# Kernel tuning notes

Hardware: AMD Instinct MI355X
Metric: run time of the kernel (lower is better)

Reference implementation:

```python
import jax, jax.numpy as jnp
import numpy as np

B, T, D, NH, FF, L, NCLS, CELL = 4, 64, 128, 4, 512, 2, 7, 64
DIMS = (600, 342, 300)


def layernorm(x, g, b, eps=1e-5):
    m = jnp.mean(x, -1, keepdims=True)
    v = jnp.mean((x - m) ** 2, -1, keepdims=True)
    return (x - m) / jnp.sqrt(v + eps) * g + b


def mha(x, Wqkv, bqkv, Wo, bo):
    N, S, Dm = x.shape
    hd = Dm // NH
    q, k, v = jnp.split(x @ Wqkv + bqkv, 3, axis=-1)
    q = q.reshape(N, S, NH, hd).transpose(0, 2, 1, 3) / jnp.float32(hd) ** 0.5
    k = k.reshape(N, S, NH, hd).transpose(0, 2, 1, 3)
    v = v.reshape(N, S, NH, hd).transpose(0, 2, 1, 3)
    att = jax.nn.softmax(jnp.einsum('nhqd,nhkd->nhqk', q, k), axis=-1)
    o = jnp.einsum('nhqk,nhkd->nhqd', att, v).transpose(0, 2, 1, 3).reshape(N, S, Dm)
    return o @ Wo + bo


def _l2norm(x):
    return x / jnp.maximum(jnp.linalg.norm(x, axis=-1, keepdims=True), 1e-12)


def _model(x_text, x_vis, x_aud, Wp_text, bp_text, Wp_vis, bp_vis, Wp_aud, bp_aud,
           lang1, lang2, Wl1, bl1, Wl2, bl2, phase_text, phase_vis, phase_aud,
           t_Wqkv, t_bqkv, t_Wo, t_bo, t_g1, t_b1, t_W1, t_bf1, t_W2, t_bf2, t_g2, t_b2,
           meas_r, meas_i, fc_W1, fc_b1, fc_W2, fc_b2):
    b, t = x_text.shape[0], x_text.shape[1]
    # modality projections + ReLU
    reps = [jax.nn.relu(x @ W + bb) for x, W, bb in
            ((x_text, Wp_text, bp_text), (x_vis, Wp_vis, bp_vis), (x_aud, Wp_aud, bp_aud))]
    l1 = jnp.broadcast_to(lang1, (b, t, lang1.shape[-1]))
    l2 = jnp.broadcast_to(lang2, (b, t, lang2.shape[-1]))
    lrep1 = jax.nn.relu(l1 @ Wl1 + bl1)
    lrep2 = jax.nn.relu(l2 @ Wl2 + bl2)
    amps = [_l2norm(r) for r in reps]
    lamp1, lamp2 = _l2norm(lrep1), _l2norm(lrep2)
    # phase embedding: smask is all-ones so index is always 0 -> single learned phase vector
    phases = [jnp.broadcast_to(p, (b, t, D)) for p in (phase_text, phase_vis, phase_aud)]
    cmul = lambda ph, a: (a * jnp.cos(ph), a * jnp.sin(ph))
    pure = [cmul(ph, a) for ph, a in zip(phases, amps)]
    ls1 = cmul(phases[0], lamp1)
    ls2 = cmul(phases[0], lamp2)
    # Hadamard gate analog on (real, imag)
    s2 = jnp.float32(2.0) ** -0.5
    h1 = ((ls1[0] + ls1[1]) * s2, (ls1[0] - ls1[1]) * s2)
    h2 = ((ls2[0] + ls2[1]) * s2, (ls2[0] - ls2[1]) * s2)
    # CNOT-style entanglement: complex elementwise product, renormalized to a pure state
    er = h1[0] * h2[0] - h1[1] * h2[1]
    ei = h1[0] * h2[1] + h1[1] * h2[0]
    en = jnp.maximum(jnp.sqrt(jnp.sum(er * er + ei * ei, -1, keepdims=True)), 1e-12)
    ent = (er / en, ei / en)

    def outer(st):  # rho = v v^dagger, v = r + i*im
        r, i = st
        rr = jnp.einsum('btd,bte->btde', r, r) + jnp.einsum('btd,bte->btde', i, i)
        ri = jnp.einsum('btd,bte->btde', i, r) - jnp.einsum('btd,bte->btde', r, i)
        return rr, ri

    mats = [outer(s) for s in pure] + [outer(ent)]
    w = jnp.concatenate([jnp.linalg.norm(r, axis=-1, keepdims=True)
                         for r in reps + [lrep1]], -1)
    w = jax.nn.softmax(w, -1)  # [B,T,4]
    rho_r = sum(w[..., m:m + 1, None] * mats[m][0] for m in range(4))
    rho_i = sum(w[..., m:m + 1, None] * mats[m][1] for m in range(4))
    # seq blocks: same block applied independently per timestep to real and imag parts
    # -> vectorize the Python loop over T (and the real/imag pair) into one batch dim
    x = jnp.concatenate([rho_r, rho_i], 0).reshape(2 * b * t, D, D)
    for l in range(L):
        x = layernorm(x + mha(x, t_Wqkv[l], t_bqkv[l], t_Wo[l], t_bo[l]), t_g1[l], t_b1[l])
        x = layernorm(x + (jax.nn.relu(x @ t_W1[l] + t_bf1[l]) @ t_W2[l] + t_bf2[l]),
                      t_g2[l], t_b2[l])
    x = x.reshape(2, b, t, D, D)
    rho_r, rho_i = x[0], x[1]
    # quantum measurement: p_k = Re(v_k^dagger rho v_k), v_k normalized complex vectors
    mn = jnp.maximum(jnp.sqrt(jnp.sum(meas_r ** 2 + meas_i ** 2, -1, keepdims=True)), 1e-12)
    vr, vi = meas_r / mn, meas_i / mn  # [K=D, D]
    ar = jnp.einsum('btde,ke->btkd', rho_r, vr) - jnp.einsum('btde,ke->btkd', rho_i, vi)
    ai = jnp.einsum('btde,ke->btkd', rho_r, vi) + jnp.einsum('btde,ke->btkd', rho_i, vr)
    probs = jnp.einsum('kd,btkd->btk', vr, ar) + jnp.einsum('kd,btkd->btk', vi, ai)
    logits = jax.nn.relu(probs @ fc_W1 + fc_b1) @ fc_W2 + fc_b2
    return jax.nn.log_softmax(logits, -1)  # [B,T,NCLS]


def setup_inputs():
    key = jax.random.key(0)
    ks = iter(jax.random.split(key, 32))
    rn = lambda shape, s=0.05: jax.random.normal(next(ks), shape, dtype=jnp.float32) * s
    z = lambda shape: jnp.zeros(shape, jnp.float32)
    o = lambda shape: jnp.ones(shape, jnp.float32)
    return dict(
        x_text=rn((B, T, DIMS[0]), 1.0), x_vis=rn((B, T, DIMS[1]), 1.0), x_aud=rn((B, T, DIMS[2]), 1.0),
        Wp_text=rn((DIMS[0], D)), bp_text=z((D,)),
        Wp_vis=rn((DIMS[1], D)), bp_vis=z((D,)),
        Wp_aud=rn((DIMS[2], D)), bp_aud=z((D,)),
        lang1=rn((1, 1, DIMS[2]), 1.0), lang2=rn((1, 1, DIMS[2]), 1.0),
        Wl1=rn((DIMS[2], D)), bl1=z((D,)), Wl2=rn((DIMS[2], D)), bl2=z((D,)),
        phase_text=rn((D,), 1.0), phase_vis=rn((D,), 1.0), phase_aud=rn((D,), 1.0),
        t_Wqkv=rn((L, D, 3 * D)), t_bqkv=z((L, 3 * D)),
        t_Wo=rn((L, D, D)), t_bo=z((L, D)),
        t_g1=o((L, D)), t_b1=z((L, D)),
        t_W1=rn((L, D, FF)), t_bf1=z((L, FF)),
        t_W2=rn((L, FF, D)), t_bf2=z((L, D)),
        t_g2=o((L, D)), t_b2=z((L, D)),
        meas_r=rn((D, D), 1.0), meas_i=rn((D, D), 1.0),
        fc_W1=rn((D, CELL)), fc_b1=z((CELL,)), fc_W2=rn((CELL, NCLS)), fc_b2=z((NCLS,)),
    )


def reference(x_text, x_vis, x_aud, Wp_text, bp_text, Wp_vis, bp_vis, Wp_aud, bp_aud,
              lang1, lang2, Wl1, bl1, Wl2, bl2, phase_text, phase_vis, phase_aud,
              t_Wqkv, t_bqkv, t_Wo, t_bo, t_g1, t_b1, t_W1, t_bf1, t_W2, t_bf2, t_g2, t_b2,
              meas_r, meas_i, fc_W1, fc_b1, fc_W2, fc_b2):
    return _model(x_text, x_vis, x_aud, Wp_text, bp_text, Wp_vis, bp_vis, Wp_aud, bp_aud,
                  lang1, lang2, Wl1, bl1, Wl2, bl2, phase_text, phase_vis, phase_aud,
                  t_Wqkv, t_bqkv, t_Wo, t_bo, t_g1, t_b1, t_W1, t_bf1, t_W2, t_bf2, t_g2, t_b2,
                  meas_r, meas_i, fc_W1, fc_b1, fc_W2, fc_b2)
```

## Files before the change

kernel.cpp:

```cpp
#include <hip/hip_runtime.h>
#include <hip/hip_bf16.h>

typedef __hip_bfloat16 bf16;
typedef short short8 __attribute__((ext_vector_type(8)));
typedef float f32x4 __attribute__((ext_vector_type(4)));

__device__ __forceinline__ float b2f(bf16 v){ return __bfloat162float(v); }

__device__ __forceinline__ short f2bs(float f){
  union { __hip_bfloat16 b; short s; } u; u.b = __float2bfloat16(f); return u.s;
}
__device__ __forceinline__ float bs2f(short s){
  union { short s; __hip_bfloat16 b; } u; u.s = s; return __bfloat162float(u.b);
}

__device__ __forceinline__ float wred_sum(float v){
  #pragma unroll
  for (int o = 32; o > 0; o >>= 1) v += __shfl_xor(v, o, 64);
  return v;
}

__device__ __forceinline__ void gload_lds16(const void* g, void* l){
  __builtin_amdgcn_global_load_lds((const __attribute__((address_space(1))) unsigned*)g,
                                   (__attribute__((address_space(3))) unsigned*)l, 16, 0, 0);
}

__device__ __forceinline__ unsigned swzA(unsigned a){ return a ^ (((a >> 8) & 7u) << 4); }
__device__ __forceinline__ unsigned swzB(unsigned a){ return a ^ (((a >> 7) & 3u) << 4); }

template<int DIMN>
__device__ void modality(const float* x, const float* W, const float* bia, const float* ph,
                         float* PURE, float* RNORM, int m, int bt, float* xs, float* red)
{
  int tid = threadIdx.x;
  for (int i = tid; i < DIMN; i += 128) xs[i] = x[bt*DIMN + i];
  __syncthreads();
  float a0 = 0.f, a1 = 0.f, a2 = 0.f, a3 = 0.f;
  int k = 0;
  for (; k + 4 <= DIMN; k += 4){
    a0 = fmaf(xs[k],   W[(k  )*128 + tid], a0);
    a1 = fmaf(xs[k+1], W[(k+1)*128 + tid], a1);
    a2 = fmaf(xs[k+2], W[(k+2)*128 + tid], a2);
    a3 = fmaf(xs[k+3], W[(k+3)*128 + tid], a3);
  }
  for (; k < DIMN; k++) a0 = fmaf(xs[k], W[k*128 + tid], a0);
  float acc = bia[tid] + ((a0 + a1) + (a2 + a3));
  float rep = fmaxf(acc, 0.f);
  float s = wred_sum(rep*rep);
  int wid = tid >> 6, lane = tid & 63;
  if (lane == 0) red[wid] = s;
  __syncthreads();
  float nrm = sqrtf(red[0] + red[1]);
  float amp = rep / fmaxf(nrm, 1e-12f);
  float p = ph[tid];
  PURE[bt*768 + m*128 + tid]       = amp * cosf(p);
  PURE[bt*768 + (3+m)*128 + tid]   = amp * sinf(p);
  if (tid == 0) RNORM[bt*4 + m] = nrm;
}

__global__ void prep_kernel(
    const float* __restrict__ Wqkv, const float* __restrict__ Wo,
    const float* __restrict__ W1, const float* __restrict__ W2,
    short* __restrict__ WqkvT, short* __restrict__ WoT,
    short* __restrict__ W1T, short* __restrict__ W2T,
    const float* xt, const float* xv, const float* xa,
    const float* Wpt, const float* bpt, const float* Wpv, const float* bpv,
    const float* Wpa, const float* bpa,
    const float* pht, const float* phv, const float* pha,
    float* PURE, float* RNORM,
    const float* l1, const float* l2,
    const float* Wl1, const float* bl1, const float* Wl2, const float* bl2,
    float* LANGB,
    const float* mr, const float* mi, float* VMEAS, short* VMEASB)
{
  __shared__ float xs[600];
  __shared__ float xs2a[300];
  __shared__ float red[4];
  int b = blockIdx.x, tid = threadIdx.x;

  if (b < 384){
    int l = b / 192, bb = b - l*192;
    const float* in; short* out; int K, N, boff;
    bool isW2 = false;
    if (bb < 48)      { in = Wqkv; out = WqkvT; K = 128; N = 384; boff = bb; }
    else if (bb < 64) { in = Wo;   out = WoT;   K = 128; N = 128; boff = bb - 48; }
    else if (bb < 128){ in = W1;   out = W1T;   K = 128; N = 512; boff = bb - 64; }
    else              { in = W2;   out = W2T;   K = 512; N = 128; boff = bb - 128; isW2 = true; }
    int base = l * K * N;
    int i0 = boff * 1024;
    #pragma unroll
    for (int t = 0; t < 8; t++){
      int i = i0 + t*128 + tid;
      if (i < K*N){
        int nn = i / K, kk = i - nn*K;
        int oi = isW2 ? ((kk >> 5)*4096 + nn*32 + (kk & 31)) : i;
        out[base + oi] = f2bs(in[base + kk*N + nn]);
      }
    }
    return;
  }
  if (b < 1152){
    int idx = b - 384;
    int bt = idx & 255, m = idx >> 8;
    if (m == 0)      modality<600>(xt, Wpt, bpt, pht, PURE, RNORM, 0, bt, xs, red);
    else if (m == 1) modality<342>(xv, Wpv, bpv, phv, PURE, RNORM, 1, bt, xs, red);
    else             modality<300>(xa, Wpa, bpa, pha, PURE, RNORM, 2, bt, xs, red);
    return;
  }
  if (b >= 1153){
    int k = b - 1153;
    float a = mr[k*128 + tid], bb2 = mi[k*128 + tid];
    float ws = wred_sum(a*a + bb2*bb2);
    int wid = tid >> 6, lane = tid & 63;
    if (lane == 0) red[wid] = ws;
    __syncthreads();
    float inv = 1.f / fmaxf(sqrtf(red[0] + red[1]), 1e-12f);
    float vr = a * inv, vi = bb2 * inv;
    int i = k*128 + tid;
    VMEAS[i]          = vr;
    VMEAS[16384 + i]  = vi;
    VMEASB[i]         = f2bs(vr);
    VMEASB[16384 + i] = f2bs(vi);
    VMEASB[32768 + i] = f2bs(-vi);
    return;
  }
  for (int i = tid; i < 300; i += 128){ xs[i] = l1[i]; xs2a[i] = l2[i]; }
  __syncthreads();
  float p10=0,p11=0,p12=0,p13=0, p20=0,p21=0,p22=0,p23=0;
  for (int k = 0; k < 300; k += 4){
    p10 = fmaf(xs[k],    Wl1[(k  )*128+tid], p10);
    p11 = fmaf(xs[k+1],  Wl1[(k+1)*128+tid], p11);
    p12 = fmaf(xs[k+2],  Wl1[(k+2)*128+tid], p12);
    p13 = fmaf(xs[k+3],  Wl1[(k+3)*128+tid], p13);
    p20 = fmaf(xs2a[k],  Wl2[(k  )*128+tid], p20);
    p21 = fmaf(xs2a[k+1],Wl2[(k+1)*128+tid], p21);
    p22 = fmaf(xs2a[k+2],Wl2[(k+2)*128+tid], p22);
    p23 = fmaf(xs2a[k+3],Wl2[(k+3)*128+tid], p23);
  }
  float a1 = bl1[tid] + ((p10+p11)+(p12+p13));
  float a2 = bl2[tid] + ((p20+p21)+(p22+p23));
  a1 = fmaxf(a1, 0.f); a2 = fmaxf(a2, 0.f);
  int wid = tid >> 6, lane = tid & 63;
  float s1 = wred_sum(a1*a1), s2 = wred_sum(a2*a2);
  if (lane == 0){ red[wid] = s1; red[2+wid] = s2; }
  __syncthreads();
  float n1 = sqrtf(red[0] + red[1]);
  float n2 = sqrtf(red[2] + red[3]);
  float lamp1 = a1 / fmaxf(n1, 1e-12f);
  float lamp2 = a2 / fmaxf(n2, 1e-12f);
  float ph = pht[tid];
  float c = cosf(ph), s = sinf(ph);
  const float s2c = 0.70710678118654752f;
  float h1r = (lamp1*c + lamp1*s)*s2c, h1i = (lamp1*c - lamp1*s)*s2c;
  float h2r = (lamp2*c + lamp2*s)*s2c, h2i = (lamp2*c - lamp2*s)*s2c;
  float er = h1r*h2r - h1i*h2i;
  float ei = h1r*h2i + h1i*h2r;
  __syncthreads();
  float se = wred_sum(er*er + ei*ei);
  if (lane == 0) red[wid] = se;
  __syncthreads();
  float en = fmaxf(sqrtf(red[0] + red[1]), 1e-12f);
  LANGB[tid]       = er / en;
  LANGB[128 + tid] = ei / en;
  if (tid == 0) LANGB[256] = n1;
}

__global__ __launch_bounds__(256) void rho_kernel(const float* PURE, const float* RNORM,
                                                  const float* LANGB, short* Xb)
{
  __shared__ float rv[4][128], iv[4][128], wsm[4];
  int bt = blockIdx.x >> 1, half = blockIdx.x & 1;
  int tid = threadIdx.x;
  for (int i = tid; i < 1024; i += 256){
    int d = i & 127;
    if (i < 768){ int m = i >> 7; float v = PURE[bt*768 + i];
                  if (m < 3) rv[m][d] = v; else iv[m-3][d] = v; }
    else if (i < 896) rv[3][d] = LANGB[d];
    else              iv[3][d] = LANGB[128 + d];
  }
  if (tid == 0){
    float n0 = RNORM[bt*4+0], n1 = RNORM[bt*4+1], n2 = RNORM[bt*4+2], n3 = LANGB[256];
    float mx = fmaxf(fmaxf(n0, n1), fmaxf(n2, n3));
    float e0 = __expf(n0-mx), e1 = __expf(n1-mx), e2 = __expf(n2-mx), e3 = __expf(n3-mx);
    float inv = 1.f / (e0+e1+e2+e3);
    wsm[0]=e0*inv; wsm[1]=e1*inv; wsm[2]=e2*inv; wsm[3]=e3*inv;
  }
  __syncthreads();
  float w0 = wsm[0], w1 = wsm[1], w2 = wsm[2], w3 = wsm[3];
  int lo = half*8192, hi = lo + 8192;
  for (int idx = lo + tid; idx < hi; idx += 256){
    int d = idx >> 7, e = idx & 127;
    float rr = 0.f, ri = 0.f;
    {
      float rd=rv[0][d], re=rv[0][e], id=iv[0][d], ie=iv[0][e];
      rr = fmaf(w0, rd*re + id*ie, rr); ri = fmaf(w0, id*re - rd*ie, ri);
    }{
      float rd=rv[1][d], re=rv[1][e], id=iv[1][d], ie=iv[1][e];
      rr = fmaf(w1, rd*re + id*ie, rr); ri = fmaf(w1, id*re - rd*ie, ri);
    }{
      float rd=rv[2][d], re=rv[2][e], id=iv[2][d], ie=iv[2][e];
      rr = fmaf(w2, rd*re + id*ie, rr); ri = fmaf(w2, id*re - rd*ie, ri);
    }{
      float rd=rv[3][d], re=rv[3][e], id=iv[3][d], ie=iv[3][e];
      rr = fmaf(w3, rd*re + id*ie, rr); ri = fmaf(w3, id*re - rd*ie, ri);
    }
    Xb[(size_t)bt*16384 + idx]        = f2bs(rr);
    Xb[(size_t)(256+bt)*16384 + idx]  = f2bs(ri);
  }
}

__global__ __launch_bounds__(256) void attn_kernel(const short* __restrict__ Xb,
    const short* __restrict__ WqkvT, const float* __restrict__ bqkv,
    bf16* __restrict__ ATTO)
{
  __shared__ __align__(16) char lds_raw[43520];
  short* Vt = (short*)(lds_raw);
  short* Qs = (short*)(lds_raw + 8704);
  short* Ks = (short*)(lds_raw + 18944);
  short* Ps = (short*)(lds_raw + 8704);

  const int n = blockIdx.x, h = blockIdx.y;
  const int tid = threadIdx.x;
  const int wid = tid >> 6, lane = tid & 63;
  const int l15 = lane & 15, quad = lane >> 4;
  const int wb = __builtin_amdgcn_readfirstlane(wid);
  const short* xn = Xb + (size_t)n*16384;
  const char* Wbase = (const char*)WqkvT;

  short8 afr[2][4];
  #pragma unroll
  for (int mi = 0; mi < 2; mi++)
    #pragma unroll
    for (int ks = 0; ks < 4; ks++){
      int row = (wid*2 + mi)*16 + l15;
      afr[mi][ks] = *(const short8*)(xn + row*128 + ks*32 + quad*8);
    }
  #pragma unroll
  for (int j = 0; j < 6; j++){
    int seg = wb*6 + j;
    int slab = seg >> 3;
    unsigned off = (unsigned)((seg & 7)*1024);
    unsigned gbase = (unsigned)((slab*128 + h*32)*256);
    gload_lds16(Wbase + gbase + swzA(off + (unsigned)(lane*16)),
                lds_raw + seg*1024);
  }
  __syncthreads();

  f32x4 acc[2][6];
  #pragma unroll
  for (int mi = 0; mi < 2; mi++)
    #pragma unroll
    for (int nt = 0; nt < 6; nt++){
      f32x4 z = {0.f, 0.f, 0.f, 0.f}; acc[mi][nt] = z;
    }

  #pragma unroll
  for (int ks = 0; ks < 4; ks++){
    #pragma unroll
    for (int nt = 0; nt < 6; nt++){
      int slab = nt >> 1;
      int col = (nt & 1)*16 + l15;
      unsigned a = (unsigned)(col*256 + ks*64 + quad*16);
      short8 bfr = *(const short8*)(lds_raw + slab*8192 + swzA(a));
      #pragma unroll
      for (int mi = 0; mi < 2; mi++)
        acc[mi][nt] = __builtin_amdgcn_mfma_f32_16x16x32_bf16(afr[mi][ks], bfr, acc[mi][nt], 0, 0, 0);
    }
  }
  __syncthreads();

  #pragma unroll
  for (int nt = 0; nt < 6; nt++){
    int sec = nt >> 1;
    int cl = (nt & 1)*16 + l15;
    float bias = bqkv[sec*128 + h*32 + cl];
    #pragma unroll
    for (int mi = 0; mi < 2; mi++){
      int rowb = (wid*2 + mi)*16 + quad*4;
      #pragma unroll
      for (int r = 0; r < 4; r++){
        float v = acc[mi][nt][r] + bias;
        int row = rowb + r;
        if (sec == 0)      Qs[row*40 + cl] = f2bs(v * 0.17677669529663687f);
        else if (sec == 1) Ks[row*40 + cl] = f2bs(v);
        else               Vt[cl*136 + row] = f2bs(v);
      }
    }
  }
  __syncthreads();

  f32x4 s[2][8];
  {
    short8 qf[2];
    #pragma unroll
    for (int mi = 0; mi < 2; mi++){
      int row = (wid*2 + mi)*16 + l15;
      qf[mi] = *(const short8*)(Qs + row*40 + quad*8);
    }
    #pragma unroll
    for (int nt = 0; nt < 8; nt++){
      int kr = nt*16 + l15;
      short8 kf = *(const short8*)(Ks + kr*40 + quad*8);
      #pragma unroll
      for (int mi = 0; mi < 2; mi++){
        f32x4 z = {0.f, 0.f, 0.f, 0.f};
        s[mi][nt] = __builtin_amdgcn_mfma_f32_16x16x32_bf16(qf[mi], kf, z, 0, 0, 0);
      }
    }
  }

  #pragma unroll
  for (int mi = 0; mi < 2; mi++){
    #pragma unroll
    for (int r = 0; r < 4; r++){
      float m = -1e30f;
      #pragma unroll
      for (int nt = 0; nt < 8; nt++) m = fmaxf(m, s[mi][nt][r]);
      #pragma unroll
      for (int o = 1; o < 16; o <<= 1) m = fmaxf(m, __shfl_xor(m, o, 64));
      float sum = 0.f;
      #pragma unroll
      for (int nt = 0; nt < 8; nt++){
        float p = __expf(s[mi][nt][r] - m);
        s[mi][nt][r] = p; sum += p;
      }
      #pragma unroll
      for (int o = 1; o < 16; o <<= 1) sum += __shfl_xor(sum, o, 64);
      float inv = 1.f / sum;
      #pragma unroll
      for (int nt = 0; nt < 8; nt++) s[mi][nt][r] *= inv;
    }
  }
  __syncthreads();

  #pragma unroll
  for (int mi = 0; mi < 2; mi++){
    int rowb = (wid*2 + mi)*16 + quad*4;
    #pragma unroll
    for (int nt = 0; nt < 8; nt++){
      int col = nt*16 + l15;
      #pragma unroll
      for (int r = 0; r < 4; r++)
        Ps[(rowb + r)*136 + col] = f2bs(s[mi][nt][r]);
    }
  }
  __syncthreads();

  f32x4 o_[2][2];
  #pragma unroll
  for (int mi = 0; mi < 2; mi++)
    #pragma unroll
    for (int n2 = 0; n2 < 2; n2++){
      f32x4 z = {0.f, 0.f, 0.f, 0.f}; o_[mi][n2] = z;
    }
  #pragma unroll
  for (int ks = 0; ks < 4; ks++){
    short8 pf[2];
    #pragma unroll
    for (int mi = 0; mi < 2; mi++){
      int row = (wid*2 + mi)*16 + l15;
      pf[mi] = *(const short8*)(Ps + row*136 + ks*32 + quad*8);
    }
    #pragma unroll
    for (int n2 = 0; n2 < 2; n2++){
      short8 vf = *(const short8*)(Vt + (n2*16 + l15)*136 + ks*32 + quad*8);
      #pragma unroll
      for (int mi = 0; mi < 2; mi++)
        o_[mi][n2] = __builtin_amdgcn_mfma_f32_16x16x32_bf16(pf[mi], vf, o_[mi][n2], 0, 0, 0);
    }
  }
  bf16* on = ATTO + (size_t)n*16384;
  #pragma unroll
  for (int mi = 0; mi < 2; mi++){
    int rowb = (wid*2 + mi)*16 + quad*4;
    #pragma unroll
    for (int n2 = 0; n2 < 2; n2++){
      int col = h*32 + n2*16 + l15;
      #pragma unroll
      for (int r = 0; r < 4; r++)
        on[(rowb + r)*128 + col] = __float2bfloat16(o_[mi][n2][r]);
    }
  }
}

__global__ __launch_bounds__(256, 2) void proj_ffn_kernel(const bf16* __restrict__ SRC,
    short* __restrict__ Xb, const short* __restrict__ WoT,
    const float* __restrict__ bo, const float* __restrict__ g1v,
    const float* __restrict__ bb1,
    const short* __restrict__ W1T, const float* __restrict__ bf1,
    const short* __restrict__ W2C, const float* __restrict__ bf2,
    const float* __restrict__ g2v, const float* __restrict__ bb2)
{
  __shared__ __align__(16) char lds_raw[65536];
  const int n = blockIdx.x, tid = threadIdx.x;
  const int wid = tid >> 6, lane = tid & 63;
  const int l15 = lane & 15, quad = lane >> 4;
  const int wb = __builtin_amdgcn_readfirstlane(wid);
  const short* an = (const short*)SRC + (size_t)n*16384;
  short* xn = Xb + (size_t)n*16384;
  char* XsB = lds_raw + 32768;
  short* Hs = (short*)(lds_raw + 32768);

  short8 af[2][4];
  #pragma unroll
  for (int mi = 0; mi < 2; mi++)
    #pragma unroll
    for (int ks = 0; ks < 4; ks++){
      int row = wid*32 + mi*16 + l15;
      af[mi][ks] = *(const short8*)(an + row*128 + ks*32 + quad*8);
    }
  #pragma unroll
  for (int j = 0; j < 8; j++){
    unsigned L = (unsigned)(j*4096 + wb*1024 + lane*16);
    gload_lds16((const char*)WoT + swzA(L), lds_raw + (j*4096 + wb*1024));
    gload_lds16((const char*)xn  + swzA(L), XsB + (j*4096 + wb*1024));
  }
  float bov[8], g1a[8], b1a[8];
  #pragma unroll
  for (int nt = 0; nt < 8; nt++){
    int col = nt*16 + l15;
    bov[nt] = bo[col]; g1a[nt] = g1v[col]; b1a[nt] = bb1[col];
  }
  __syncthreads();

  f32x4 Y[2][8];
  #pragma unroll
  for (int mi = 0; mi < 2; mi++)
    #pragma unroll
    for (int nt = 0; nt < 8; nt++){ f32x4 z = {0.f,0.f,0.f,0.f}; Y[mi][nt] = z; }
  #pragma unroll
  for (int ks = 0; ks < 4; ks++){
    #pragma unroll
    for (int nt = 0; nt < 8; nt++){
      unsigned a = (unsigned)((nt*16 + l15)*256 + ks*64 + quad*16);
      short8 bh = *(const short8*)(lds_raw + swzA(a));
      #pragma unroll
      for (int mi = 0; mi < 2; mi++)
        Y[mi][nt] = __builtin_amdgcn_mfma_f32_16x16x32_bf16(af[mi][ks], bh, Y[mi][nt], 0, 0, 0);
    }
  }
  __syncthreads();

  #pragma unroll
  for (int j = 0; j < 2; j++){
    unsigned L = (unsigned)(j*4096 + wb*1024 + lane*16);
    gload_lds16((const char*)W1T + swzA(L), lds_raw + (j*4096 + wb*1024));
    gload_lds16((const char*)W2C + swzB(L), lds_raw + (8192 + j*4096 + wb*1024));
  }

  unsigned yv1p[2][4][4];
  #pragma unroll
  for (int mi = 0; mi < 2; mi++){
    #pragma unroll
    for (int r = 0; r < 4; r++){
      int row = wid*32 + mi*16 + quad*4 + r;
      float yv[8]; float S = 0.f, Q = 0.f;
      #pragma unroll
      for (int nt = 0; nt < 8; nt++){
        int col = nt*16 + l15;
        float res = bs2f(*(const short*)(XsB + swzA((unsigned)(row*256 + col*2))));
        float y = Y[mi][nt][r] + bov[nt] + res;
        yv[nt] = y; S += y; Q += y*y;
      }
      #pragma unroll
      for (int o = 1; o < 16; o <<= 1){ S += __shfl_xor(S, o, 64); Q += __shfl_xor(Q, o, 64); }
      float m = S * (1.f/128.f);
      float var = Q * (1.f/128.f) - m*m;
      float inv = rsqrtf(var + 1e-5f);
      #pragma unroll
      for (int nt = 0; nt < 8; nt++){
        int col = nt*16 + l15;
        short ob = f2bs((yv[nt] - m) * inv * g1a[nt] + b1a[nt]);
        *(short*)(XsB + swzA((unsigned)(row*256 + col*2))) = ob;
        unsigned u = (unsigned)(unsigned short)ob;
        if ((nt & 1) == 0) yv1p[mi][r][nt>>1] = u;
        else               yv1p[mi][r][nt>>1] |= (u << 16);
      }
    }
  }

  short8 af2[2][4];
  #pragma unroll
  for (int mi = 0; mi < 2; mi++)
    #pragma unroll
    for (int ks = 0; ks < 4; ks++){
      int row = wid*32 + mi*16 + l15;
      unsigned a = (unsigned)(row*256 + ks*64 + quad*16);
      af2[mi][ks] = *(const short8*)(XsB + swzA(a));
    }
  __syncthreads();

  f32x4 Y2[2][8];
  #pragma unroll
  for (int mi = 0; mi < 2; mi++)
    #pragma unroll
    for (int nt = 0; nt < 8; nt++){ f32x4 z = {0.f,0.f,0.f,0.f}; Y2[mi][nt] = z; }

  for (int c = 0; c < 16; c++){
    const int cb = c & 1;
    if (c < 15){
      const int nb = cb ^ 1;
      #pragma unroll
      for (int j = 0; j < 2; j++){
        unsigned L = (unsigned)(j*4096 + wb*1024 + lane*16);
        gload_lds16((const char*)W1T + (unsigned)((c+1)*8192) + swzA(L),
                    lds_raw + (nb*16384 + j*4096 + wb*1024));
        gload_lds16((const char*)W2C + (unsigned)((c+1)*8192) + swzB(L),
                    lds_raw + (nb*16384 + 8192 + j*4096 + wb*1024));
      }
    }
    const char* bW1 = lds_raw + cb*16384;
    const char* bW2 = lds_raw + cb*16384 + 8192;

    f32x4 Hc[2][2];
    #pragma unroll
    for (int mi = 0; mi < 2; mi++)
      #pragma unroll
      for (int nt2 = 0; nt2 < 2; nt2++){ f32x4 z = {0.f,0.f,0.f,0.f}; Hc[mi][nt2] = z; }
    #pragma unroll
    for (int ks = 0; ks < 4; ks++){
      #pragma unroll
      for (int nt2 = 0; nt2 < 2; nt2++){
        unsigned a = (unsigned)((nt2*16 + l15)*256 + ks*64 + quad*16);
        short8 bh = *(const short8*)(bW1 + swzA(a));
        #pragma unroll
        for (int mi = 0; mi < 2; mi++)
          Hc[mi][nt2] = __builtin_amdgcn_mfma_f32_16x16x32_bf16(af2[mi][ks], bh, Hc[mi][nt2], 0, 0, 0);
      }
    }
    float b1v0 = bf1[c*32 + l15];
    float b1v1 = bf1[c*32 + 16 + l15];
    #pragma unroll
    for (int nt2 = 0; nt2 < 2; nt2++){
      int col = nt2*16 + l15;
      float b1v = nt2 ? b1v1 : b1v0;
      #pragma unroll
      for (int mi = 0; mi < 2; mi++){
        int rowb = wid*32 + mi*16 + quad*4;
        #pragma unroll
        for (int r = 0; r < 4; r++)
          Hs[(rowb + r)*40 + col] = f2bs(fmaxf(Hc[mi][nt2][r] + b1v, 0.f));
      }
    }
    short8 ph[2];
    #pragma unroll
    for (int mi = 0; mi < 2; mi++){
      int row = wid*32 + mi*16 + l15;
      ph[mi] = *(const short8*)(Hs + row*40 + quad*8);
    }
    #pragma unroll
    for (int nt = 0; nt < 8; nt++){
      unsigned a = (unsigned)((nt*16 + l15)*64 + quad*16);
      short8 bh = *(const short8*)(bW2 + swzB(a));
      #pragma unroll
      for (int mi = 0; mi < 2; mi++)
        Y2[mi][nt] = __builtin_amdgcn_mfma_f32_16x16x32_bf16(ph[mi], bh, Y2[mi][nt], 0, 0, 0);
    }
    if (c < 15) __syncthreads();
  }

  {
    float b2v[8], gv[8], bbv[8];
    #pragma unroll
    for (int nt = 0; nt < 8; nt++){
      int col = nt*16 + l15;
      b2v[nt] = bf2[col]; gv[nt] = g2v[col]; bbv[nt] = bb2[col];
    }
    #pragma unroll
    for (int mi = 0; mi < 2; mi++){
      #pragma unroll
      for (int r = 0; r < 4; r++){
        int row = wid*32 + mi*16 + quad*4 + r;
        float yv[8]; float S = 0.f, Q = 0.f;
        #pragma unroll
        for (int nt = 0; nt < 8; nt++){
          unsigned u = yv1p[mi][r][nt>>1];
          short rs = (short)((nt & 1) ? (u >> 16) : (u & 0xffffu));
          float y = Y2[mi][nt][r] + b2v[nt] + bs2f(rs);
          yv[nt] = y; S += y; Q += y*y;
        }
        #pragma unroll
        for (int o = 1; o < 16; o <<= 1){ S += __shfl_xor(S, o, 64); Q += __shfl_xor(Q, o, 64); }
        float m = S * (1.f/128.f);
        float var = Q * (1.f/128.f) - m*m;
        float inv = rsqrtf(var + 1e-5f);
        #pragma unroll
        for (int nt = 0; nt < 8; nt++){
          int col = nt*16 + l15;
          xn[row*128 + col] = f2bs((yv[nt] - m) * inv * gv[nt] + bbv[nt]);
        }
      }
    }
  }
}

__global__ __launch_bounds__(256) void probs_kernel(const short* __restrict__ Xb,
    const float* __restrict__ VMEAS, const short* __restrict__ VMEASB,
    float* __restrict__ PROBS)
{
  __shared__ __align__(16) char lds_raw[24576];
  __shared__ float sp[128];
  const int bt = blockIdx.x, z = blockIdx.y, tid = threadIdx.x;
  const int wid = tid >> 6, lane = tid & 63;
  const int l15 = lane & 15, quad = lane >> 4;
  const int wb = __builtin_amdgcn_readfirstlane(wid);
  const short* R = Xb + (size_t)bt*16384;
  const short* I = Xb + (size_t)(256+bt)*16384;

  if (tid < 128) sp[tid] = 0.f;

  const int drow = z*64 + wid*16 + l15;
  short8 aR[4], aI[4];
  #pragma unroll
  for (int ks = 0; ks < 4; ks++){
    aR[ks] = *(const short8*)(R + drow*128 + ks*32 + quad*8);
    aI[ks] = *(const short8*)(I + drow*128 + ks*32 + quad*8);
  }

  #define STAGE_NT(nt_, buf_)                                                  \
    { _Pragma("unroll")                                                        \
      for (int j = 0; j < 3; j++){                                             \
        int seg = wb*3 + j;                                         \
        int s = seg >> 2;                                       \
        unsigned off = (unsigned)((seg & 3)*1024);                             \
        gload_lds16((const char*)VMEASB + s*32768 + (nt_)*4096 +               \
                      swzA(off + (unsigned)(lane*16)),                         \
                    lds_raw + (buf_)*12288 + s*4096 + (int)off);               \
      } }

  STAGE_NT(0, 0)
  __syncthreads();

  const int db = z*64 + wid*16 + quad*4;

  for (int nt = 0; nt < 8; nt++){
    const int cb = nt & 1;
    if (nt < 7) STAGE_NT(nt+1, cb^1)

    const char* bvr = lds_raw + cb*12288;
    const char* bvi = bvr + 4096;
    const char* bnv = bvr + 8192;

    f32x4 Ar = {0.f,0.f,0.f,0.f}, Ai = {0.f,0.f,0.f,0.f};
    #pragma unroll
    for (int ks = 0; ks < 4; ks++){
      unsigned a = swzA((unsigned)(l15*256 + ks*64 + quad*16));
      short8 b_vr = *(const short8*)(bvr + a);
      short8 b_vi = *(const short8*)(bvi + a);
      short8 b_nv = *(const short8*)(bnv + a);
      Ar = __builtin_amdgcn_mfma_f32_16x16x32_bf16(aR[ks], b_vr, Ar, 0, 0, 0);
      Ar = __builtin_amdgcn_mfma_f32_16x16x32_bf16(aI[ks], b_nv, Ar, 0, 0, 0);
      Ai = __builtin_amdgcn_mfma_f32_16x16x32_bf16(aR[ks], b_vi, Ai, 0, 0, 0);
      Ai = __builtin_amdgcn_mfma_f32_16x16x32_bf16(aI[ks], b_vr, Ai, 0, 0, 0);
    }

    int k = nt*16 + l15;
    f32x4 vR = *(const f32x4*)(VMEAS + k*128 + db);
    f32x4 vI = *(const f32x4*)(VMEAS + 16384 + k*128 + db);
    float pv = 0.f;
    #pragma unroll
    for (int r = 0; r < 4; r++) pv += vR[r]*Ar[r] + vI[r]*Ai[r];

    pv += __shfl_xor(pv, 16, 64);
    pv += __shfl_xor(pv, 32, 64);
    if (quad == 0) atomicAdd(&sp[nt*16 + l15], pv);

    __syncthreads();
  }
  #undef STAGE_NT

  if (tid < 128) PROBS[(size_t)(z*256 + bt)*128 + tid] = sp[tid];
}

__global__ void head_kernel(const float* PROBS, const float* W1, const float* b1,
                            const float* W2, const float* b2, float* out)
{
  __shared__ float h[64];
  __shared__ float lg[7];
  __shared__ float mred[2];
  int bt = blockIdx.x, tid = threadIdx.x;
  float a0 = b1[tid], a1 = 0.f, a2 = 0.f, a3 = 0.f;
  for (int d = 0; d < 128; d += 4){
    float p0 = PROBS[bt*128 + d  ] + PROBS[(256+bt)*128 + d  ];
    float p1 = PROBS[bt*128 + d+1] + PROBS[(256+bt)*128 + d+1];
    float p2 = PROBS[bt*128 + d+2] + PROBS[(256+bt)*128 + d+2];
    float p3 = PROBS[bt*128 + d+3] + PROBS[(256+bt)*128 + d+3];
    a0 = fmaf(p0, W1[(d  )*64 + tid], a0);
    a1 = fmaf(p1, W1[(d+1)*64 + tid], a1);
    a2 = fmaf(p2, W1[(d+2)*64 + tid], a2);
    a3 = fmaf(p3, W1[(d+3)*64 + tid], a3);
  }
  h[tid] = fmaxf((a0 + a1) + (a2 + a3), 0.f);
  __syncthreads();
  if (tid < 7){
    float a = b2[tid];
    for (int j = 0; j < 64; j++) a = fmaf(h[j], W2[j*7 + tid], a);
    lg[tid] = a;
  }
  __syncthreads();
  if (tid == 0){
    float M = -1e30f;
    for (int c = 0; c < 7; c++) M = fmaxf(M, lg[c]);
    float S = 0.f;
    for (int c = 0; c < 7; c++) S += __expf(lg[c] - M);
    mred[0] = M; mred[1] = logf(S);
  }
  __syncthreads();
  if (tid < 7) out[bt*7 + tid] = lg[tid] - mred[0] - mred[1];
}

extern "C" void kernel_launch(void* const* d_in, const int* in_sizes, int n_in,
                              void* d_out, int out_size, void* d_ws, size_t ws_size,
                              hipStream_t stream)
{
  (void)in_sizes; (void)n_in; (void)out_size; (void)ws_size;
  const float* xt   = (const float*)d_in[0];
  const float* xv   = (const float*)d_in[1];
  const float* xa   = (const float*)d_in[2];
  const float* Wpt  = (const float*)d_in[3];
  const float* bpt  = (const float*)d_in[4];
  const float* Wpv  = (const float*)d_in[5];
  const float* bpv  = (const float*)d_in[6];
  const float* Wpa  = (const float*)d_in[7];
  const float* bpa  = (const float*)d_in[8];
  const float* l1   = (const float*)d_in[9];
  const float* l2   = (const float*)d_in[10];
  const float* Wl1  = (const float*)d_in[11];
  const float* bl1  = (const float*)d_in[12];
  const float* Wl2  = (const float*)d_in[13];
  const float* bl2  = (const float*)d_in[14];
  const float* pht  = (const float*)d_in[15];
  const float* phv  = (const float*)d_in[16];
  const float* pha  = (const float*)d_in[17];
  const float* Wqkv = (const float*)d_in[18];
  const float* bqkv = (const float*)d_in[19];
  const float* Wo   = (const float*)d_in[20];
  const float* bo   = (const float*)d_in[21];
  const float* g1   = (const float*)d_in[22];
  const float* b1   = (const float*)d_in[23];
  const float* W1   = (const float*)d_in[24];
  const float* bf1  = (const float*)d_in[25];
  const float* W2   = (const float*)d_in[26];
  const float* bf2  = (const float*)d_in[27];
  const float* g2   = (const float*)d_in[28];
  const float* b2   = (const float*)d_in[29];
  const float* mr   = (const float*)d_in[30];
  const float* mi   = (const float*)d_in[31];
  const float* fcW1 = (const float*)d_in[32];
  const float* fcb1 = (const float*)d_in[33];
  const float* fcW2 = (const float*)d_in[34];
  const float* fcb2 = (const float*)d_in[35];
  float* out = (float*)d_out;

  char* wsb = (char*)d_ws;
  short* Xb     = (short*)(wsb);
  bf16*  ATTO   = (bf16*) (wsb + 16777216);
  float* PURE   = (float*)(wsb + 33554432);
  float* RNORM  = (float*)(wsb + 34340864);
  float* LANGB  = (float*)(wsb + 34344960);
  float* VMEAS  = (float*)(wsb + 34347008);
  float* PROBS  = (float*)(wsb + 34478080);
  short* WqkvT  = (short*)(wsb + 34740224);
  short* WoT    = (short*)(wsb + 34936832);
  short* W1T    = (short*)(wsb + 35002368);
  short* W2T    = (short*)(wsb + 35264512);
  short* VMEASB = (short*)(wsb + 35526656);

  prep_kernel<<<1281, 128, 0, stream>>>(Wqkv, Wo, W1, W2, WqkvT, WoT, W1T, W2T,
                                        xt, xv, xa, Wpt, bpt, Wpv, bpv, Wpa, bpa,
                                        pht, phv, pha, PURE, RNORM,
                                        l1, l2, Wl1, bl1, Wl2, bl2, LANGB,
                                        mr, mi, VMEAS, VMEASB);

  rho_kernel<<<512, 256, 0, stream>>>(PURE, RNORM, LANGB, Xb);

  for (int l = 0; l < 2; l++){
    attn_kernel<<<dim3(512, 4), 256, 0, stream>>>(Xb, WqkvT + (size_t)l*49152,
                                                  bqkv + (size_t)l*384, ATTO);
    proj_ffn_kernel<<<512, 256, 0, stream>>>(ATTO, Xb,
                                             WoT + (size_t)l*16384,
                                             bo + (size_t)l*128, g1 + (size_t)l*128,
                                             b1 + (size_t)l*128,
                                             W1T + (size_t)l*65536, bf1 + (size_t)l*512,
                                             W2T + (size_t)l*65536, bf2 + (size_t)l*128,
                                             g2 + (size_t)l*128, b2 + (size_t)l*128);
  }

  probs_kernel<<<dim3(256, 2), 256, 0, stream>>>(Xb, VMEAS, VMEASB, PROBS);
  head_kernel<<<256, 64, 0, stream>>>(PROBS, fcW1, fcb1, fcW2, fcb2, out);
}
```

Measured before the change: 290.6 us.

## Tile weight transpose, fuse probs with head, tighten FFN pipeline waits

The weight-transpose prep now goes through a 32x33 shared-memory tile, so both the global reads and the writes are coalesced. The probs and head kernels are merged into one launch: each block covers both 64-row halves and feeds the MLP head straight from shared memory, which removes the PROBS round trip and one launch. In the FFN chunk loop and the probs loop, __syncthreads is replaced by explicit vmcnt waits plus raw s_barrier so prefetches overlap compute, and bf1 is cached in LDS. The hand-written vmcnt counts must match the number of outstanding loads exactly, or the code can read stale LDS data.

Measured after the change: 289.8 us. Within noise of the previous version (-0.3%).

```diff
diff --git a/kernel.cpp b/kernel.cpp
--- a/kernel.cpp
+++ b/kernel.cpp
@@ -76,26 +76,34 @@
   __shared__ float xs[600];
   __shared__ float xs2a[300];
   __shared__ float red[4];
+  __shared__ float tile[32][33];
   int b = blockIdx.x, tid = threadIdx.x;
 
   if (b < 384){
     int l = b / 192, bb = b - l*192;
-    const float* in; short* out; int K, N, boff;
+    const float* in; short* out; int K, N, kt, nt_;
     bool isW2 = false;
-    if (bb < 48)      { in = Wqkv; out = WqkvT; K = 128; N = 384; boff = bb; }
-    else if (bb < 64) { in = Wo;   out = WoT;   K = 128; N = 128; boff = bb - 48; }
-    else if (bb < 128){ in = W1;   out = W1T;   K = 128; N = 512; boff = bb - 64; }
-    else              { in = W2;   out = W2T;   K = 512; N = 128; boff = bb - 128; isW2 = true; }
+    if (bb < 48)      { in = Wqkv; out = WqkvT; K = 128; N = 384; kt = bb & 3;  nt_ = bb >> 2; }
+    else if (bb < 64) { int t = bb-48;  in = Wo; out = WoT; K = 128; N = 128; kt = t & 3;  nt_ = t >> 2; }
+    else if (bb < 128){ int t = bb-64;  in = W1; out = W1T; K = 128; N = 512; kt = t & 3;  nt_ = t >> 2; }
+    else              { int t = bb-128; in = W2; out = W2T; K = 512; N = 128; kt = t & 15; nt_ = t >> 4; isW2 = true; }
     int base = l * K * N;
-    int i0 = boff * 1024;
-    #pragma unroll
-    for (int t = 0; t < 8; t++){
-      int i = i0 + t*128 + tid;
-      if (i < K*N){
-        int nn = i / K, kk = i - nn*K;
-        int oi = isW2 ? ((kk >> 5)*4096 + nn*32 + (kk & 31)) : i;
-        out[base + oi] = f2bs(in[base + kk*N + nn]);
-      }
+    int kk0 = kt*32, nn0 = nt_*32;
+    int r0 = tid >> 5, c = tid & 31;
+    #pragma unroll
+    for (int i = 0; i < 8; i++){
+      int r = i*4 + r0;
+      tile[r][c] = in[base + (kk0 + r)*N + nn0 + c];
+    }
+    __syncthreads();
+    #pragma unroll
+    for (int i = 0; i < 8; i++){
+      int rr = i*4 + r0;
+      float v = tile[c][rr];
+      int oi;
+      if (!isW2) oi = (nn0 + rr)*K + kk0 + c;
+      else       oi = kt*4096 + (nn0 + rr)*32 + c;
+      out[base + oi] = f2bs(v);
     }
     return;
   }
@@ -392,6 +400,7 @@
     const float* __restrict__ g2v, const float* __restrict__ bb2)
 {
   __shared__ __align__(16) char lds_raw[65536];
+  __shared__ float bf1L[512];
   const int n = blockIdx.x, tid = threadIdx.x;
   const int wid = tid >> 6, lane = tid & 63;
   const int l15 = lane & 15, quad = lane >> 4;
@@ -415,6 +424,7 @@
     gload_lds16((const char*)WoT + swzA(L), lds_raw + (j*4096 + wb*1024));
     gload_lds16((const char*)xn  + swzA(L), XsB + (j*4096 + wb*1024));
   }
+  for (int i = tid; i < 512; i += 256) bf1L[i] = bf1[i];
   float bov[8], g1a[8], b1a[8];
   #pragma unroll
   for (int nt = 0; nt < 8; nt++){
@@ -508,7 +518,14 @@
         gload_lds16((const char*)W2C + (unsigned)((c+1)*8192) + swzB(L),
                     lds_raw + (nb*16384 + 8192 + j*4096 + wb*1024));
       }
-    }
+      asm volatile("s_waitcnt vmcnt(4)" ::: "memory");
+    } else {
+      asm volatile("s_waitcnt vmcnt(0)" ::: "memory");
+    }
+    __builtin_amdgcn_sched_barrier(0);
+    __builtin_amdgcn_s_barrier();
+    __builtin_amdgcn_sched_barrier(0);
+
     const char* bW1 = lds_raw + cb*16384;
     const char* bW2 = lds_raw + cb*16384 + 8192;
 
@@ -528,8 +545,8 @@
           Hc[mi][nt2] = __builtin_amdgcn_mfma_f32_16x16x32_bf16(af2[mi][ks], bh, Hc[mi][nt2], 0, 0, 0);
       }
     }
-    float b1v0 = bf1[c*32 + l15];
-    float b1v1 = bf1[c*32 + 16 + l15];
+    float b1v0 = bf1L[c*32 + l15];
+    float b1v1 = bf1L[c*32 + 16 + l15];
     #pragma unroll
     for (int nt2 = 0; nt2 < 2; nt2++){
       int col = nt2*16 + l15;
@@ -556,7 +573,9 @@
       for (int mi = 0; mi < 2; mi++)
         Y2[mi][nt] = __builtin_amdgcn_mfma_f32_16x16x32_bf16(ph[mi], bh, Y2[mi][nt], 0, 0, 0);
     }
-    if (c < 15) __syncthreads();
+    __builtin_amdgcn_sched_barrier(0);
+    __builtin_amdgcn_s_barrier();
+    __builtin_amdgcn_sched_barrier(0);
   }
 
   {
@@ -594,13 +613,18 @@
   }
 }
 
-__global__ __launch_bounds__(256) void probs_kernel(const short* __restrict__ Xb,
+__global__ __launch_bounds__(256) void probs_head_kernel(const short* __restrict__ Xb,
     const float* __restrict__ VMEAS, const short* __restrict__ VMEASB,
-    float* __restrict__ PROBS)
+    const float* __restrict__ W1, const float* __restrict__ b1,
+    const float* __restrict__ W2, const float* __restrict__ b2,
+    float* __restrict__ out)
 {
   __shared__ __align__(16) char lds_raw[24576];
   __shared__ float sp[128];
-  const int bt = blockIdx.x, z = blockIdx.y, tid = threadIdx.x;
+  __shared__ float hsh[64];
+  __shared__ float lg[7];
+  __shared__ float mred[2];
+  const int bt = blockIdx.x, tid = threadIdx.x;
   const int wid = tid >> 6, lane = tid & 63;
   const int l15 = lane & 15, quad = lane >> 4;
   const int wb = __builtin_amdgcn_readfirstlane(wid);
@@ -609,12 +633,15 @@
 
   if (tid < 128) sp[tid] = 0.f;
 
-  const int drow = z*64 + wid*16 + l15;
-  short8 aR[4], aI[4];
-  #pragma unroll
-  for (int ks = 0; ks < 4; ks++){
-    aR[ks] = *(const short8*)(R + drow*128 + ks*32 + quad*8);
-    aI[ks] = *(const short8*)(I + drow*128 + ks*32 + quad*8);
+  short8 aR[2][4], aI[2][4];
+  #pragma unroll
+  for (int z = 0; z < 2; z++){
+    int drow = z*64 + wid*16 + l15;
+    #pragma unroll
+    for (int ks = 0; ks < 4; ks++){
+      aR[z][ks] = *(const short8*)(R + drow*128 + ks*32 + quad*8);
+      aI[z][ks] = *(const short8*)(I + drow*128 + ks*32 + quad*8);
+    }
   }
 
   #define STAGE_NT(nt_, buf_)                                                  \
@@ -631,70 +658,78 @@
   STAGE_NT(0, 0)
   __syncthreads();
 
-  const int db = z*64 + wid*16 + quad*4;
+  const int db0 = wid*16 + quad*4;
 
   for (int nt = 0; nt < 8; nt++){
     const int cb = nt & 1;
-    if (nt < 7) STAGE_NT(nt+1, cb^1)
+    int k = nt*16 + l15;
+    f32x4 vR0 = *(const f32x4*)(VMEAS + k*128 + db0);
+    f32x4 vI0 = *(const f32x4*)(VMEAS + 16384 + k*128 + db0);
+    f32x4 vR1 = *(const f32x4*)(VMEAS + k*128 + 64 + db0);
+    f32x4 vI1 = *(const f32x4*)(VMEAS + 16384 + k*128 + 64 + db0);
+    if (nt < 7){
+      STAGE_NT(nt+1, cb^1)
+      asm volatile("s_waitcnt vmcnt(3)" ::: "memory");
+    } else {
+      asm volatile("s_waitcnt vmcnt(0)" ::: "memory");
+    }
+    __builtin_amdgcn_sched_barrier(0);
+    __builtin_amdgcn_s_barrier();
+    __builtin_amdgcn_sched_barrier(0);
 
     const char* bvr = lds_raw + cb*12288;
     const char* bvi = bvr + 4096;
     const char* bnv = bvr + 8192;
 
-    f32x4 Ar = {0.f,0.f,0.f,0.f}, Ai = {0.f,0.f,0.f,0.f};
+    f32x4 Ar0 = {0.f,0.f,0.f,0.f}, Ai0 = {0.f,0.f,0.f,0.f};
+    f32x4 Ar1 = {0.f,0.f,0.f,0.f}, Ai1 = {0.f,0.f,0.f,0.f};
     #pragma unroll
     for (int ks = 0; ks < 4; ks++){
       unsigned a = swzA((unsigned)(l15*256 + ks*64 + quad*16));
       short8 b_vr = *(const short8*)(bvr + a);
       short8 b_vi = *(const short8*)(bvi + a);
       short8 b_nv = *(const short8*)(bnv + a);
-      Ar = __builtin_amdgcn_mfma_f32_16x16x32_bf16(aR[ks], b_vr, Ar, 0, 0, 0);
-      Ar = __builtin_amdgcn_mfma_f32_16x16x32_bf16(aI[ks], b_nv, Ar, 0, 0, 0);
-      Ai = __builtin_amdgcn_mfma_f32_16x16x32_bf16(aR[ks], b_vi, Ai, 0, 0, 0);
-      Ai = __builtin_amdgcn_mfma_f32_16x16x32_bf16(aI[ks], b_vr, Ai, 0, 0, 0);
-    }
-
-    int k = nt*16 + l15;
-    f32x4 vR = *(const f32x4*)(VMEAS + k*128 + db);
-    f32x4 vI = *(const f32x4*)(VMEAS + 16384 + k*128 + db);
+      Ar0 = __builtin_amdgcn_mfma_f32_16x16x32_bf16(aR[0][ks], b_vr, Ar0, 0, 0, 0);
+      Ar0 = __builtin_amdgcn_mfma_f32_16x16x32_bf16(aI[0][ks], b_nv, Ar0, 0, 0, 0);
+      Ai0 = __builtin_amdgcn_mfma_f32_16x16x32_bf16(aR[0][ks], b_vi, Ai0, 0, 0, 0);
+      Ai0 = __builtin_amdgcn_mfma_f32_16x16x32_bf16(aI[0][ks], b_vr, Ai0, 0, 0, 0);
+      Ar1 = __builtin_amdgcn_mfma_f32_16x16x32_bf16(aR[1][ks], b_vr, Ar1, 0, 0, 0);
+      Ar1 = __builtin_amdgcn_mfma_f32_16x16x32_bf16(aI[1][ks], b_nv, Ar1, 0, 0, 0);
+      Ai1 = __builtin_amdgcn_mfma_f32_16x16x32_bf16(aR[1][ks], b_vi, Ai1, 0, 0, 0);
+      Ai1 = __builtin_amdgcn_mfma_f32_16x16x32_bf16(aI[1][ks], b_vr, Ai1, 0, 0, 0);
+    }
+
     float pv = 0.f;
     #pragma unroll
-    for (int r = 0; r < 4; r++) pv += vR[r]*Ar[r] + vI[r]*Ai[r];
-
+    for (int r = 0; r < 4; r++){
+      pv += vR0[r]*Ar0[r] + vI0[r]*Ai0[r];
+      pv += vR1[r]*Ar1[r] + vI1[r]*Ai1[r];
+    }
     pv += __shfl_xor(pv, 16, 64);
     pv += __shfl_xor(pv, 32, 64);
     if (quad == 0) atomicAdd(&sp[nt*16 + l15], pv);
 
-    __syncthreads();
+    __builtin_amdgcn_sched_barrier(0);
+    __builtin_amdgcn_s_barrier();
+    __builtin_amdgcn_sched_barrier(0);
   }
   #undef STAGE_NT
 
-  if (tid < 128) PROBS[(size_t)(z*256 + bt)*128 + tid] = sp[tid];
-}
-
-__global__ void head_kernel(const float* PROBS, const float* W1, const float* b1,
-                            const float* W2, const float* b2, float* out)
-{
-  __shared__ float h[64];
-  __shared__ float lg[7];
-  __shared__ float mred[2];
-  int bt = blockIdx.x, tid = threadIdx.x;
-  float a0 = b1[tid], a1 = 0.f, a2 = 0.f, a3 = 0.f;
-  for (int d = 0; d < 128; d += 4){
-    float p0 = PROBS[bt*128 + d  ] + PROBS[(256+bt)*128 + d  ];
-    float p1 = PROBS[bt*128 + d+1] + PROBS[(256+bt)*128 + d+1];
-    float p2 = PROBS[bt*128 + d+2] + PROBS[(256+bt)*128 + d+2];
-    float p3 = PROBS[bt*128 + d+3] + PROBS[(256+bt)*128 + d+3];
-    a0 = fmaf(p0, W1[(d  )*64 + tid], a0);
-    a1 = fmaf(p1, W1[(d+1)*64 + tid], a1);
-    a2 = fmaf(p2, W1[(d+2)*64 + tid], a2);
-    a3 = fmaf(p3, W1[(d+3)*64 + tid], a3);
-  }
-  h[tid] = fmaxf((a0 + a1) + (a2 + a3), 0.f);
+  __syncthreads();
+  if (tid < 64){
+    float a0 = b1[tid], a1 = 0.f, a2 = 0.f, a3 = 0.f;
+    for (int d = 0; d < 128; d += 4){
+      a0 = fmaf(sp[d  ], W1[(d  )*64 + tid], a0);
+      a1 = fmaf(sp[d+1], W1[(d+1)*64 + tid], a1);
+      a2 = fmaf(sp[d+2], W1[(d+2)*64 + tid], a2);
+      a3 = fmaf(sp[d+3], W1[(d+3)*64 + tid], a3);
+    }
+    hsh[tid] = fmaxf((a0 + a1) + (a2 + a3), 0.f);
+  }
   __syncthreads();
   if (tid < 7){
     float a = b2[tid];
-    for (int j = 0; j < 64; j++) a = fmaf(h[j], W2[j*7 + tid], a);
+    for (int j = 0; j < 64; j++) a = fmaf(hsh[j], W2[j*7 + tid], a);
     lg[tid] = a;
   }
   __syncthreads();
@@ -759,7 +794,6 @@
   float* RNORM  = (float*)(wsb + 34340864);
   float* LANGB  = (float*)(wsb + 34344960);
   float* VMEAS  = (float*)(wsb + 34347008);
-  float* PROBS  = (float*)(wsb + 34478080);
   short* WqkvT  = (short*)(wsb + 34740224);
   short* WoT    = (short*)(wsb + 34936832);
   short* W1T    = (short*)(wsb + 35002368);
@@ -786,6 +820,6 @@
                                              g2 + (size_t)l*128, b2 + (size_t)l*128);
   }
 
-  probs_kernel<<<dim3(256, 2), 256, 0, stream>>>(Xb, VMEAS, VMEASB, PROBS);
-  head_kernel<<<256, 64, 0, stream>>>(PROBS, fcW1, fcb1, fcW2, fcb2, out);
-}
+  probs_head_kernel<<<256, 256, 0, stream>>>(Xb, VMEAS, VMEASB,
+                                             fcW1, fcb1, fcW2, fcb2, out);
+}
```
